# Optimization experiments

Hardware: AMD Instinct MI355X
Metric: run time of the kernel (lower is better)

The kernel has to match this reference:

```python
import jax, jax.numpy as jnp
import numpy as np

D = 1024
H = 16
HD = D // H


def setup_inputs() -> dict:
    key = jax.random.key(0)
    ks = jax.random.split(key, 9)
    s = 1.0 / np.sqrt(D)
    inp = {
        "x": jax.random.normal(ks[0], (2, 2048, D), dtype=jnp.float32),
        "Wq": jax.random.uniform(ks[1], (D, D), jnp.float32, -s, s),
        "bq": jax.random.uniform(ks[2], (D,), jnp.float32, -s, s),
        "Wk": jax.random.uniform(ks[3], (D, D), jnp.float32, -s, s),
        "bk": jax.random.uniform(ks[4], (D,), jnp.float32, -s, s),
        "Wv": jax.random.uniform(ks[5], (D, D), jnp.float32, -s, s),
        "bv": jax.random.uniform(ks[6], (D,), jnp.float32, -s, s),
        "Wo": jax.random.uniform(ks[7], (D, D), jnp.float32, -s, s),
        "bo": jax.random.uniform(ks[8], (D,), jnp.float32, -s, s),
    }
    return inp


def reference(x, Wq, bq, Wk, bk, Wv, bv, Wo, bo):
    B, S, _ = x.shape
    scale = jnp.sqrt(jnp.asarray(HD, dtype=jnp.float32))
    # QKV projections, split into heads: [B, H, S, HD]
    def proj(W, b):
        y = jnp.einsum('bsd,de->bse', x, W) + b
        return y.reshape(B, S, H, HD).transpose(0, 2, 1, 3)
    Q, K, V = proj(Wq, bq), proj(Wk, bk), proj(Wv, bv)
    scores = jnp.einsum('bhqd,bhkd->bhqk', Q, K) / scale  # [B,H,S,S]
    attn = jax.nn.softmax(scores, axis=-1)
    ctx = jnp.einsum('bhqk,bhkd->bhqd', attn, V)
    ctx = ctx.transpose(0, 2, 1, 3).reshape(B, S, D)
    return jnp.einsum('bsd,de->bse', ctx, Wo) + bo
```

## Files before the change

kernel.cpp:

```cpp
#include <hip/hip_runtime.h>
#include <hip/hip_bf16.h>

typedef __attribute__((ext_vector_type(8))) short bf16x8;
typedef __attribute__((ext_vector_type(4))) float f32x4;

constexpr int Sc  = 2048;
constexpr int Dc  = 1024;
constexpr int Hc  = 16;
constexpr int HDc = 64;
constexpr int Mc  = 4096;

constexpr float ECs = 0.18033688011112042f;

__device__ __forceinline__ ushort f2bf(float f) {
  unsigned u = __float_as_uint(f);
  u += 0x7fffu + ((u >> 16) & 1u);
  return (ushort)(u >> 16);
}
__device__ __forceinline__ float bf2f(ushort h) {
  return __uint_as_float(((unsigned)h) << 16);
}

union US8 {
  ushort u[8];
  uint   w[4];
  bf16x8 v;
};

__global__ __launch_bounds__(256) void split_x_kernel(
    const float* __restrict__ X, ushort* __restrict__ H) {
  const int i    = blockIdx.x * 256 + threadIdx.x;
  const float4 v = ((const float4*)X)[i];
  ushort4 h;
  h.x = f2bf(v.x);
  h.y = f2bf(v.y);
  h.z = f2bf(v.z);
  h.w = f2bf(v.w);
  ((ushort4*)H)[i] = h;
}

struct SplitP {
  const float* W[4];
  ushort*      Th[4];
  ushort*      Tl[4];
};

__global__ __launch_bounds__(256) void split_wt_kernel(SplitP p) {
  __shared__ float T[64][69];
  const int z = blockIdx.z;
  const float* W = p.W[z];
  const int t  = threadIdx.x;
  const int c  = (t & 15) * 4;
  const int r  = t >> 4;
  const int n0 = blockIdx.x * 64, k0 = blockIdx.y * 64;
#pragma unroll
  for (int pp = 0; pp < 4; ++pp) {
    const int k    = r + pp * 16;
    const float4 v = *(const float4*)(W + (size_t)(k0 + k) * 1024 + n0 + c);
    T[k][c + 0] = v.x;
    T[k][c + 1] = v.y;
    T[k][c + 2] = v.z;
    T[k][c + 3] = v.w;
  }
  __syncthreads();
#pragma unroll
  for (int pp = 0; pp < 4; ++pp) {
    const int n = r + pp * 16;
    const float x0 = T[c + 0][n], x1 = T[c + 1][n], x2 = T[c + 2][n], x3 = T[c + 3][n];
    ushort4 h, l;
    h.x = f2bf(x0); l.x = f2bf(x0 - bf2f(h.x));
    h.y = f2bf(x1); l.y = f2bf(x1 - bf2f(h.y));
    h.z = f2bf(x2); l.z = f2bf(x2 - bf2f(h.z));
    h.w = f2bf(x3); l.w = f2bf(x3 - bf2f(h.w));
    *(ushort4*)(p.Th[z] + (size_t)(n0 + n) * 1024 + k0 + c) = h;
    if (z != 3)
      *(ushort4*)(p.Tl[z] + (size_t)(n0 + n) * 1024 + k0 + c) = l;
  }
}

struct GemmP {
  const ushort* Bh[3];
  const ushort* Bl[3];
  const float*  bias[3];
  void*         Out[3];
};

template <bool QKV>
__global__ __launch_bounds__(256) void gemm_bf16(
    const ushort* __restrict__ A, GemmP p) {
  __shared__ __align__(16) ushort As[128 * 32];
  __shared__ __align__(16) ushort BsH[128 * 32];
  __shared__ __align__(16) ushort BsL[QKV ? 128 * 32 : 16];

  const int t  = threadIdx.x;
  const int z  = blockIdx.z;
  const int m0 = blockIdx.x * 128, n0 = blockIdx.y * 128;
  const ushort* Bh  = p.Bh[z];
  const ushort* Bl  = p.Bl[z];
  const float* bias = p.bias[z];

  const int lane = t & 63, wave = t >> 6;
  const int wm = (wave & 1) * 64, wn = (wave >> 1) * 64;

  f32x4 acc[4][4];
#pragma unroll
  for (int i = 0; i < 4; ++i)
#pragma unroll
    for (int j = 0; j < 4; ++j) acc[i][j] = (f32x4){0.f, 0.f, 0.f, 0.f};

  const int am = t >> 2;
  const int ac = t & 3;
  const ushort* gA  = A  + (size_t)(m0 + am) * 1024 + ac * 8;
  const ushort* gBh = Bh + (size_t)(n0 + am) * 1024 + ac * 8;
  const ushort* gBl = Bl + (size_t)(n0 + am) * 1024 + ac * 8;
  const int sw = ((ac + (am >> 1)) & 3) * 8;
  const int l0 = am * 32 + sw, l1 = (am + 64) * 32 + sw;

  const int fr  = lane & 15;
  const int fkb = (((lane >> 4) + (fr >> 1)) & 3) * 16;

  bf16x8 rA0, rA1, rH0, rH1, rL0, rL1;
  rA0 = *(const bf16x8*)(gA);
  rA1 = *(const bf16x8*)(gA + 64 * 1024);
  rH0 = *(const bf16x8*)(gBh);
  rH1 = *(const bf16x8*)(gBh + 64 * 1024);
  if (QKV) {
    rL0 = *(const bf16x8*)(gBl);
    rL1 = *(const bf16x8*)(gBl + 64 * 1024);
  }

  for (int k0 = 0; k0 < 1024; k0 += 32) {
    __syncthreads();
    *(bf16x8*)&As[l0]  = rA0;
    *(bf16x8*)&As[l1]  = rA1;
    *(bf16x8*)&BsH[l0] = rH0;
    *(bf16x8*)&BsH[l1] = rH1;
    if (QKV) {
      *(bf16x8*)&BsL[l0] = rL0;
      *(bf16x8*)&BsL[l1] = rL1;
    }
    __syncthreads();

    if (k0 + 32 < 1024) {
      const int kn = k0 + 32;
      rA0 = *(const bf16x8*)(gA + kn);
      rA1 = *(const bf16x8*)(gA + kn + 64 * 1024);
      rH0 = *(const bf16x8*)(gBh + kn);
      rH1 = *(const bf16x8*)(gBh + kn + 64 * 1024);
      if (QKV) {
        rL0 = *(const bf16x8*)(gBl + kn);
        rL1 = *(const bf16x8*)(gBl + kn + 64 * 1024);
      }
    }

    bf16x8 a[4], b_h[4], b_l[4];
#pragma unroll
    for (int i = 0; i < 4; ++i) {
      const int ra = (wm + i * 16 + fr) * 64 + fkb;
      const int rb = (wn + i * 16 + fr) * 64 + fkb;
      a[i]   = *(const bf16x8*)((const char*)As + ra);
      b_h[i] = *(const bf16x8*)((const char*)BsH + rb);
      if (QKV) b_l[i] = *(const bf16x8*)((const char*)BsL + rb);
    }
#pragma unroll
    for (int i = 0; i < 4; ++i)
#pragma unroll
      for (int j = 0; j < 4; ++j) {
        acc[i][j] = __builtin_amdgcn_mfma_f32_16x16x32_bf16(a[i], b_h[j], acc[i][j], 0, 0, 0);
        if (QKV)
          acc[i][j] = __builtin_amdgcn_mfma_f32_16x16x32_bf16(a[i], b_l[j], acc[i][j], 0, 0, 0);
      }
  }

  const float osc = (QKV && z == 0) ? ECs : 1.0f;
  const int cr = (lane >> 4) * 4;
  const int cc = lane & 15;
#pragma unroll
  for (int j = 0; j < 4; ++j) {
    const int n    = n0 + wn + j * 16 + cc;
    const float bv = bias[n];
#pragma unroll
    for (int i = 0; i < 4; ++i) {
      const int mb = m0 + wm + i * 16 + cr;
#pragma unroll
      for (int r = 0; r < 4; ++r) {
        const int m   = mb + r;
        const float v = (acc[i][j][r] + bv) * osc;
        if (QKV) {
          const int b = m >> 11, s = m & 2047, h = n >> 6, hd = n & 63;
          ((ushort*)p.Out[z])[(((size_t)(b * Hc + h) * Sc + s) << 6) + hd] = f2bf(v);
        } else {
          ((float*)p.Out[z])[(size_t)m * 1024 + n] = v;
        }
      }
    }
  }
}

__global__ __launch_bounds__(256) void attn_mfma3(
    const ushort* __restrict__ Q, const ushort* __restrict__ K,
    const ushort* __restrict__ V, ushort* __restrict__ CTX) {
  __shared__ __align__(16) ushort Ks[64 * 72];
  __shared__ __align__(16) ushort Vt[64 * 72];

  const int t    = threadIdx.x;
  const int lane = t & 63, wave = t >> 6;
  const int c16 = lane & 15, quad = lane >> 4;
  const int bh = blockIdx.x, qt = blockIdx.y;
  const int bb = bh >> 4, hh = bh & 15;

  const ushort* Qb = Q + (size_t)bh * Sc * HDc + (size_t)qt * 128 * HDc;
  const ushort* Kb = K + (size_t)bh * Sc * HDc;
  const ushort* Vb = V + (size_t)bh * Sc * HDc;

  bf16x8 aq[2][2];
#pragma unroll
  for (int mt = 0; mt < 2; ++mt)
#pragma unroll
    for (int c = 0; c < 2; ++c)
      aq[mt][c] = *(const bf16x8*)(Qb + (size_t)(wave * 32 + mt * 16 + c16) * 64 + c * 32 + quad * 8);

  US8 ones_u;
#pragma unroll
  for (int e = 0; e < 8; ++e) ones_u.u[e] = 0x3F80;
  const bf16x8 ones = ones_u.v;

  f32x4 ctx[2][4], lacc[2];
#pragma unroll
  for (int mt = 0; mt < 2; ++mt) {
    lacc[mt] = (f32x4){0.f, 0.f, 0.f, 0.f};
#pragma unroll
    for (int j = 0; j < 4; ++j) ctx[mt][j] = (f32x4){0.f, 0.f, 0.f, 0.f};
  }

  const int krow = t >> 2, kc = (t & 3) * 8;
  const int kg = t & 15, dg = t >> 4;
  const int lb = ((kg >> 3) << 5) | ((kg & 3) << 3) | (((kg >> 2) & 1) << 2);

  const ushort* gK = Kb + (size_t)krow * 64 + kc;
  const ushort* gV = Vb + (size_t)(kg * 4) * 64 + dg * 4;

  bf16x8 kr0, kr1;
  ushort4 vr[4];
  kr0 = *(const bf16x8*)(gK);
  kr1 = *(const bf16x8*)(gK + 32);
#pragma unroll
  for (int i = 0; i < 4; ++i) vr[i] = *(const ushort4*)(gV + (size_t)i * 64);

  for (int kt = 0; kt < 32; ++kt) {
    __syncthreads();
    *(bf16x8*)&Ks[krow * 72 + kc]      = kr0;
    *(bf16x8*)&Ks[krow * 72 + kc + 32] = kr1;
    {
      const uint* w0 = (const uint*)&vr[0];
      const uint* w1 = (const uint*)&vr[1];
      const uint* w2 = (const uint*)&vr[2];
      const uint* w3 = (const uint*)&vr[3];
#pragma unroll
      for (int j = 0; j < 4; ++j) {
        const int  wd  = j >> 1;
        const uint sel = (j & 1) ? 0x07060302u : 0x05040100u;
        const uint lo  = __builtin_amdgcn_perm(w1[wd], w0[wd], sel);
        const uint hi  = __builtin_amdgcn_perm(w3[wd], w2[wd], sel);
        *(uint2*)&Vt[(dg * 4 + j) * 72 + lb] = make_uint2(lo, hi);
      }
    }
    __syncthreads();

    if (kt < 31) {
      const size_t adv = (size_t)(kt + 1) * 64 * 64;
      kr0 = *(const bf16x8*)(gK + adv);
      kr1 = *(const bf16x8*)(gK + adv + 32);
#pragma unroll
      for (int i = 0; i < 4; ++i) vr[i] = *(const ushort4*)(gV + adv + (size_t)i * 64);
    }

    f32x4 st[2][4];
#pragma unroll
    for (int mt = 0; mt < 2; ++mt)
#pragma unroll
      for (int j = 0; j < 4; ++j) st[mt][j] = (f32x4){0.f, 0.f, 0.f, 0.f};
#pragma unroll
    for (int c = 0; c < 2; ++c)
#pragma unroll
      for (int j = 0; j < 4; ++j) {
        const bf16x8 ak = *(const bf16x8*)&Ks[(j * 16 + c16) * 72 + c * 32 + quad * 8];
        st[0][j] = __builtin_amdgcn_mfma_f32_16x16x32_bf16(ak, aq[0][c], st[0][j], 0, 0, 0);
        st[1][j] = __builtin_amdgcn_mfma_f32_16x16x32_bf16(ak, aq[1][c], st[1][j], 0, 0, 0);
      }

    US8 pf[2][2];
#pragma unroll
    for (int mt = 0; mt < 2; ++mt)
#pragma unroll
      for (int c2 = 0; c2 < 2; ++c2)
#pragma unroll
        for (int w = 0; w < 4; ++w) {
          const int jj = c2 * 2 + (w >> 1);
          const int r0 = (w & 1) * 2;
          const float pe = __builtin_amdgcn_exp2f(st[mt][jj][r0]);
          const float po = __builtin_amdgcn_exp2f(st[mt][jj][r0 + 1]);
          pf[mt][c2].w[w] = __builtin_amdgcn_perm(
              __float_as_uint(po), __float_as_uint(pe), 0x07060302u);
        }

#pragma unroll
    for (int c2 = 0; c2 < 2; ++c2) {
      lacc[0] = __builtin_amdgcn_mfma_f32_16x16x32_bf16(pf[0][c2].v, ones, lacc[0], 0, 0, 0);
      lacc[1] = __builtin_amdgcn_mfma_f32_16x16x32_bf16(pf[1][c2].v, ones, lacc[1], 0, 0, 0);
#pragma unroll
      for (int j = 0; j < 4; ++j) {
        const bf16x8 bv = *(const bf16x8*)&Vt[(j * 16 + c16) * 72 + c2 * 32 + quad * 8];
        ctx[0][j] = __builtin_amdgcn_mfma_f32_16x16x32_bf16(pf[0][c2].v, bv, ctx[0][j], 0, 0, 0);
        ctx[1][j] = __builtin_amdgcn_mfma_f32_16x16x32_bf16(pf[1][c2].v, bv, ctx[1][j], 0, 0, 0);
      }
    }
  }

#pragma unroll
  for (int mt = 0; mt < 2; ++mt) {
#pragma unroll
    for (int r = 0; r < 4; ++r) {
      const float inv = 1.f / lacc[mt][r];
      const int srow  = qt * 128 + wave * 32 + mt * 16 + quad * 4 + r;
      const size_t rb = ((size_t)(bb * Sc + srow)) * 1024 + hh * 64;
#pragma unroll
      for (int j = 0; j < 4; ++j)
        CTX[rb + j * 16 + c16] = f2bf(ctx[mt][j][r] * inv);
    }
  }
}

extern "C" void kernel_launch(void* const* d_in, const int* in_sizes, int n_in,
                              void* d_out, int out_size, void* d_ws, size_t ws_size,
                              hipStream_t stream) {
  (void)in_sizes; (void)n_in; (void)out_size; (void)ws_size;
  const float* x  = (const float*)d_in[0];
  const float* Wq = (const float*)d_in[1];
  const float* bq = (const float*)d_in[2];
  const float* Wk = (const float*)d_in[3];
  const float* bk = (const float*)d_in[4];
  const float* Wv = (const float*)d_in[5];
  const float* bv = (const float*)d_in[6];
  const float* Wo = (const float*)d_in[7];
  const float* bo = (const float*)d_in[8];

  const size_t MB = 1024 * 1024;
  char* w    = (char*)d_ws;
  ushort* Qw = (ushort*)(w + 0 * MB);
  ushort* Kw = (ushort*)(w + 8 * MB);
  ushort* Vw = (ushort*)(w + 16 * MB);
  ushort* Cw = (ushort*)(w + 24 * MB);
  ushort* Xh = (ushort*)(w + 32 * MB);
  ushort* WT = (ushort*)(w + 40 * MB);
  ushort* Whq = WT + 0 * 1048576; ushort* Wlq = WT + 1 * 1048576;
  ushort* Whk = WT + 2 * 1048576; ushort* Wlk = WT + 3 * 1048576;
  ushort* Whv = WT + 4 * 1048576; ushort* Wlv = WT + 5 * 1048576;
  ushort* Who = WT + 6 * 1048576; ushort* Wlo = WT + 7 * 1048576;

  const dim3 blk(256);

  split_x_kernel<<<4096, blk, 0, stream>>>(x, Xh);

  SplitP sp;
  sp.W[0] = Wq; sp.W[1] = Wk; sp.W[2] = Wv; sp.W[3] = Wo;
  sp.Th[0] = Whq; sp.Th[1] = Whk; sp.Th[2] = Whv; sp.Th[3] = Who;
  sp.Tl[0] = Wlq; sp.Tl[1] = Wlk; sp.Tl[2] = Wlv; sp.Tl[3] = Wlo;
  split_wt_kernel<<<dim3(16, 16, 4), blk, 0, stream>>>(sp);

  GemmP pq;
  pq.Bh[0] = Whq; pq.Bh[1] = Whk; pq.Bh[2] = Whv;
  pq.Bl[0] = Wlq; pq.Bl[1] = Wlk; pq.Bl[2] = Wlv;
  pq.bias[0] = bq; pq.bias[1] = bk; pq.bias[2] = bv;
  pq.Out[0] = Qw; pq.Out[1] = Kw; pq.Out[2] = Vw;
  gemm_bf16<true><<<dim3(Mc / 128, Dc / 128, 3), blk, 0, stream>>>(Xh, pq);

  attn_mfma3<<<dim3(2 * Hc, Sc / 128), blk, 0, stream>>>(Qw, Kw, Vw, Cw);

  GemmP po;
  po.Bh[0] = po.Bh[1] = po.Bh[2] = Who;
  po.Bl[0] = po.Bl[1] = po.Bl[2] = Wlo;
  po.bias[0] = po.bias[1] = po.bias[2] = bo;
  po.Out[0] = po.Out[1] = po.Out[2] = d_out;
  gemm_bf16<false><<<dim3(Mc / 128, Dc / 128, 1), blk, 0, stream>>>(Cw, po);
}
```

Baseline: 213.2 us.

## Load MFMA A/K fragments directly from global memory, bypassing LDS staging

The GEMM kernel no longer stages the A tile through shared memory. Each wave loads its A MFMA fragments straight from global memory into registers and prefetches the next k-slice right after its use. The output-projection GEMM switches to 64-row tiles with waves split along N, which doubles its grid. In attention, the K tile is likewise read directly into per-lane fragments instead of through LDS. This cuts LDS traffic and footprint, but each wave now issues more redundant, less coalesced global loads, and A/K data is no longer shared across waves.

```diff
diff --git a/kernel.cpp b/kernel.cpp
--- a/kernel.cpp
+++ b/kernel.cpp
@@ -88,40 +88,46 @@
 template <bool QKV>
 __global__ __launch_bounds__(256) void gemm_bf16(
     const ushort* __restrict__ A, GemmP p) {
-  __shared__ __align__(16) ushort As[128 * 32];
   __shared__ __align__(16) ushort BsH[128 * 32];
   __shared__ __align__(16) ushort BsL[QKV ? 128 * 32 : 16];
 
+  constexpr int JT    = QKV ? 4 : 2;
+  constexpr int MROWS = QKV ? 128 : 64;
+
   const int t  = threadIdx.x;
   const int z  = blockIdx.z;
-  const int m0 = blockIdx.x * 128, n0 = blockIdx.y * 128;
+  const int m0 = blockIdx.x * MROWS, n0 = blockIdx.y * 128;
   const ushort* Bh  = p.Bh[z];
   const ushort* Bl  = p.Bl[z];
   const float* bias = p.bias[z];
 
   const int lane = t & 63, wave = t >> 6;
-  const int wm = (wave & 1) * 64, wn = (wave >> 1) * 64;
-
-  f32x4 acc[4][4];
+  const int wm = QKV ? (wave & 1) * 64 : 0;
+  const int wn = QKV ? (wave >> 1) * 64 : wave * 32;
+
+  f32x4 acc[4][JT];
 #pragma unroll
   for (int i = 0; i < 4; ++i)
 #pragma unroll
-    for (int j = 0; j < 4; ++j) acc[i][j] = (f32x4){0.f, 0.f, 0.f, 0.f};
+    for (int j = 0; j < JT; ++j) acc[i][j] = (f32x4){0.f, 0.f, 0.f, 0.f};
 
   const int am = t >> 2;
   const int ac = t & 3;
-  const ushort* gA  = A  + (size_t)(m0 + am) * 1024 + ac * 8;
   const ushort* gBh = Bh + (size_t)(n0 + am) * 1024 + ac * 8;
   const ushort* gBl = Bl + (size_t)(n0 + am) * 1024 + ac * 8;
   const int sw = ((ac + (am >> 1)) & 3) * 8;
   const int l0 = am * 32 + sw, l1 = (am + 64) * 32 + sw;
 
-  const int fr  = lane & 15;
-  const int fkb = (((lane >> 4) + (fr >> 1)) & 3) * 16;
-
-  bf16x8 rA0, rA1, rH0, rH1, rL0, rL1;
-  rA0 = *(const bf16x8*)(gA);
-  rA1 = *(const bf16x8*)(gA + 64 * 1024);
+  const int fr   = lane & 15;
+  const int quad = lane >> 4;
+  const int fkb  = ((quad + (fr >> 1)) & 3) * 16;
+
+  const ushort* gA = A + (size_t)(m0 + wm + fr) * 1024 + quad * 8;
+
+  bf16x8 fa[4];
+#pragma unroll
+  for (int i = 0; i < 4; ++i) fa[i] = *(const bf16x8*)(gA + i * 16 * 1024);
+  bf16x8 rH0, rH1, rL0, rL1;
   rH0 = *(const bf16x8*)(gBh);
   rH1 = *(const bf16x8*)(gBh + 64 * 1024);
   if (QKV) {
@@ -131,8 +137,6 @@
 
   for (int k0 = 0; k0 < 1024; k0 += 32) {
     __syncthreads();
-    *(bf16x8*)&As[l0]  = rA0;
-    *(bf16x8*)&As[l1]  = rA1;
     *(bf16x8*)&BsH[l0] = rH0;
     *(bf16x8*)&BsH[l1] = rH1;
     if (QKV) {
@@ -141,10 +145,9 @@
     }
     __syncthreads();
 
-    if (k0 + 32 < 1024) {
-      const int kn = k0 + 32;
-      rA0 = *(const bf16x8*)(gA + kn);
-      rA1 = *(const bf16x8*)(gA + kn + 64 * 1024);
+    const int  kn   = k0 + 32;
+    const bool more = kn < 1024;
+    if (more) {
       rH0 = *(const bf16x8*)(gBh + kn);
       rH1 = *(const bf16x8*)(gBh + kn + 64 * 1024);
       if (QKV) {
@@ -153,30 +156,30 @@
       }
     }
 
-    bf16x8 a[4], b_h[4], b_l[4];
+    bf16x8 b_h[JT], b_l[JT];
+#pragma unroll
+    for (int j = 0; j < JT; ++j) {
+      const int rb = (wn + j * 16 + fr) * 64 + fkb;
+      b_h[j] = *(const bf16x8*)((const char*)BsH + rb);
+      if (QKV) b_l[j] = *(const bf16x8*)((const char*)BsL + rb);
+    }
 #pragma unroll
     for (int i = 0; i < 4; ++i) {
-      const int ra = (wm + i * 16 + fr) * 64 + fkb;
-      const int rb = (wn + i * 16 + fr) * 64 + fkb;
-      a[i]   = *(const bf16x8*)((const char*)As + ra);
-      b_h[i] = *(const bf16x8*)((const char*)BsH + rb);
-      if (QKV) b_l[i] = *(const bf16x8*)((const char*)BsL + rb);
-    }
-#pragma unroll
-    for (int i = 0; i < 4; ++i)
-#pragma unroll
-      for (int j = 0; j < 4; ++j) {
-        acc[i][j] = __builtin_amdgcn_mfma_f32_16x16x32_bf16(a[i], b_h[j], acc[i][j], 0, 0, 0);
+#pragma unroll
+      for (int j = 0; j < JT; ++j) {
+        acc[i][j] = __builtin_amdgcn_mfma_f32_16x16x32_bf16(fa[i], b_h[j], acc[i][j], 0, 0, 0);
         if (QKV)
-          acc[i][j] = __builtin_amdgcn_mfma_f32_16x16x32_bf16(a[i], b_l[j], acc[i][j], 0, 0, 0);
-      }
+          acc[i][j] = __builtin_amdgcn_mfma_f32_16x16x32_bf16(fa[i], b_l[j], acc[i][j], 0, 0, 0);
+      }
+      if (more) fa[i] = *(const bf16x8*)(gA + kn + i * 16 * 1024);
+    }
   }
 
   const float osc = (QKV && z == 0) ? ECs : 1.0f;
-  const int cr = (lane >> 4) * 4;
-  const int cc = lane & 15;
-#pragma unroll
-  for (int j = 0; j < 4; ++j) {
+  const int cr = quad * 4;
+  const int cc = fr;
+#pragma unroll
+  for (int j = 0; j < JT; ++j) {
     const int n    = n0 + wn + j * 16 + cc;
     const float bv = bias[n];
 #pragma unroll
@@ -197,10 +200,9 @@
   }
 }
 
-__global__ __launch_bounds__(256) void attn_mfma3(
+__global__ __launch_bounds__(256) void attn_mfma4(
     const ushort* __restrict__ Q, const ushort* __restrict__ K,
     const ushort* __restrict__ V, ushort* __restrict__ CTX) {
-  __shared__ __align__(16) ushort Ks[64 * 72];
   __shared__ __align__(16) ushort Vt[64 * 72];
 
   const int t    = threadIdx.x;
@@ -233,24 +235,24 @@
     for (int j = 0; j < 4; ++j) ctx[mt][j] = (f32x4){0.f, 0.f, 0.f, 0.f};
   }
 
-  const int krow = t >> 2, kc = (t & 3) * 8;
   const int kg = t & 15, dg = t >> 4;
   const int lb = ((kg >> 3) << 5) | ((kg & 3) << 3) | (((kg >> 2) & 1) << 2);
-
-  const ushort* gK = Kb + (size_t)krow * 64 + kc;
   const ushort* gV = Vb + (size_t)(kg * 4) * 64 + dg * 4;
 
-  bf16x8 kr0, kr1;
+  const ushort* gKf = Kb + (size_t)c16 * 64 + quad * 8;
+
+  bf16x8 fk[2][4];
+#pragma unroll
+  for (int c = 0; c < 2; ++c)
+#pragma unroll
+    for (int j = 0; j < 4; ++j)
+      fk[c][j] = *(const bf16x8*)(gKf + j * 16 * 64 + c * 32);
   ushort4 vr[4];
-  kr0 = *(const bf16x8*)(gK);
-  kr1 = *(const bf16x8*)(gK + 32);
 #pragma unroll
   for (int i = 0; i < 4; ++i) vr[i] = *(const ushort4*)(gV + (size_t)i * 64);
 
   for (int kt = 0; kt < 32; ++kt) {
     __syncthreads();
-    *(bf16x8*)&Ks[krow * 72 + kc]      = kr0;
-    *(bf16x8*)&Ks[krow * 72 + kc + 32] = kr1;
     {
       const uint* w0 = (const uint*)&vr[0];
       const uint* w1 = (const uint*)&vr[1];
@@ -269,8 +271,6 @@
 
     if (kt < 31) {
       const size_t adv = (size_t)(kt + 1) * 64 * 64;
-      kr0 = *(const bf16x8*)(gK + adv);
-      kr1 = *(const bf16x8*)(gK + adv + 32);
 #pragma unroll
       for (int i = 0; i < 4; ++i) vr[i] = *(const ushort4*)(gV + adv + (size_t)i * 64);
     }
@@ -284,10 +284,18 @@
     for (int c = 0; c < 2; ++c)
 #pragma unroll
       for (int j = 0; j < 4; ++j) {
-        const bf16x8 ak = *(const bf16x8*)&Ks[(j * 16 + c16) * 72 + c * 32 + quad * 8];
-        st[0][j] = __builtin_amdgcn_mfma_f32_16x16x32_bf16(ak, aq[0][c], st[0][j], 0, 0, 0);
-        st[1][j] = __builtin_amdgcn_mfma_f32_16x16x32_bf16(ak, aq[1][c], st[1][j], 0, 0, 0);
-      }
+        st[0][j] = __builtin_amdgcn_mfma_f32_16x16x32_bf16(fk[c][j], aq[0][c], st[0][j], 0, 0, 0);
+        st[1][j] = __builtin_amdgcn_mfma_f32_16x16x32_bf16(fk[c][j], aq[1][c], st[1][j], 0, 0, 0);
+      }
+
+    if (kt < 31) {
+      const size_t adv = (size_t)(kt + 1) * 64 * 64;
+#pragma unroll
+      for (int c = 0; c < 2; ++c)
+#pragma unroll
+        for (int j = 0; j < 4; ++j)
+          fk[c][j] = *(const bf16x8*)(gKf + adv + j * 16 * 64 + c * 32);
+    }
 
     US8 pf[2][2];
 #pragma unroll
@@ -375,12 +383,12 @@
   pq.Out[0] = Qw; pq.Out[1] = Kw; pq.Out[2] = Vw;
   gemm_bf16<true><<<dim3(Mc / 128, Dc / 128, 3), blk, 0, stream>>>(Xh, pq);
 
-  attn_mfma3<<<dim3(2 * Hc, Sc / 128), blk, 0, stream>>>(Qw, Kw, Vw, Cw);
+  attn_mfma4<<<dim3(2 * Hc, Sc / 128), blk, 0, stream>>>(Qw, Kw, Vw, Cw);
 
   GemmP po;
   po.Bh[0] = po.Bh[1] = po.Bh[2] = Who;
   po.Bl[0] = po.Bl[1] = po.Bl[2] = Wlo;
   po.bias[0] = po.bias[1] = po.bias[2] = bo;
   po.Out[0] = po.Out[1] = po.Out[2] = d_out;
-  gemm_bf16<false><<<dim3(Mc / 128, Dc / 128, 1), blk, 0, stream>>>(Cw, po);
-}
+  gemm_bf16<false><<<dim3(Mc / 64, Dc / 128, 1), blk, 0, stream>>>(Cw, po);
+}
```

New measurement: 292.8 us. +37.4%, slower.
